# Performance work log

Hardware: AMD Instinct MI355X
Metric: run time of the kernel (lower is better)

The kernel has to match this reference:

```python
import jax, jax.numpy as jnp
import numpy as np

B, S, K, N, NO = 2, 4096, 4096, 4096, 32


def setup_inputs() -> dict:
    key = jax.random.key(0)
    k0, k1, k2, k3 = jax.random.split(key, 4)
    # activations with a few high-magnitude 'outlier' columns (LLM.int8-style)
    x = jax.random.normal(k0, (B, S, K), dtype=jnp.float16)
    ind = jnp.sort(jax.random.randint(k1, (NO,), 0, K)).astype(jnp.int32)
    x = x.at[:, :, ind].multiply(jnp.float16(30.0))
    # fp16 master weight -> quantize exactly as the module's init path does
    w = (jax.random.normal(k2, (N, K), dtype=jnp.float32) * 0.02)
    weight_cache = w[:, ind].astype(jnp.float16)          # original outlier cols
    w_z = w.at[:, ind].set(0.0)                            # zero outlier cols
    scale = (jnp.max(jnp.abs(w_z), axis=1) / 127.0)        # per-out-channel scale
    q_weight = jnp.clip(jnp.round(w_z / scale[:, None]), -128.0, 127.0).astype(jnp.int8)
    bias = (jax.random.normal(k3, (N,), dtype=jnp.float32) * 0.01)
    # packed (N, 2): [:, 0] = dequant scale, [:, 1] = bias (matches q_scale_col layout)
    scale_col = jnp.stack([scale, bias], axis=1).astype(jnp.float16)
    return {
        "x": x,
        "q_weight": q_weight,
        "scale_col": scale_col,
        "weight_cache": weight_cache,
        "ind": ind,
    }


def reference(x, q_weight, scale_col, weight_cache, ind):
    # mixgemmforward_dynamic: per-row dynamic activation quant, int8 GEMM,
    # per-(row,col) dequant, fused bias add, fp16 outlier-column correction.
    Bx, Sx, Kx = x.shape
    Nx = q_weight.shape[0]
    xf = x.astype(jnp.float32).reshape(-1, Kx)                    # [M, K]
    scale_row = jnp.max(jnp.abs(xf), axis=1, keepdims=True) / 127.0  # [M, 1]
    q_x = jnp.round(jnp.clip(xf / scale_row, -128.0, 127.0))      # int-valued f32
    acc = q_x @ q_weight.astype(jnp.float32).T                    # [M, N] int GEMM
    w_scale = scale_col[:, 0].astype(jnp.float32)                 # [N]
    bias = scale_col[:, 1].astype(jnp.float32)                    # [N]
    y = acc * scale_row * w_scale[None, :] + bias[None, :]
    # outlier correction: fp16 GEMM over the extracted outlier columns
    y = y + xf[:, ind] @ weight_cache.astype(jnp.float32).T
    return y.reshape(Bx, Sx, Nx).astype(jnp.float16)
```

## Files before the change

### kernel.cpp

```cpp
#include <hip/hip_runtime.h>
#include <stdint.h>


typedef float    f32x4  __attribute__((ext_vector_type(4)));
typedef int      i32x4  __attribute__((ext_vector_type(4)));
typedef _Float16 half8  __attribute__((ext_vector_type(8)));
typedef _Float16 half4  __attribute__((ext_vector_type(4)));

#define MTOT 8192
#define NTOT 4096
#define KTOT 4096

#define SWZ(r) (((r) >> 1) & 3)

static __device__ __forceinline__ void gload16(const int8_t* g, int8_t* l) {
  __builtin_amdgcn_global_load_lds(
      (const __attribute__((address_space(1))) void*)g,
      (__attribute__((address_space(3))) void*)l, 16, 0, 0);
}

__global__ __launch_bounds__(256) void pack_kernel(
    const int* __restrict__ qw32, int8_t* __restrict__ qw8,
    const float* __restrict__ wc, _Float16* __restrict__ wch)
{
  const int bid = blockIdx.x;
  const int t = threadIdx.x;
  if (bid < 4096) {
    const int base = bid * 4096;
#pragma unroll
    for (int g = 0; g < 4; ++g) {
      const int off = g * 1024 + t * 4;
      const i32x4 v = *(const i32x4*)(qw32 + base + off);
      const uint32_t o = (uint32_t)(v[0] & 255) | ((uint32_t)(v[1] & 255) << 8) |
                         ((uint32_t)(v[2] & 255) << 16) | ((uint32_t)(v[3] & 255) << 24);
      *(uint32_t*)(qw8 + base + off) = o;
    }
  } else {
    const int idx = (bid - 4096) * 1024 + t * 4;
    const float4 v = *(const float4*)(wc + idx);
    half4 h = {(_Float16)v.x, (_Float16)v.y, (_Float16)v.z, (_Float16)v.w};
    *(half4*)(wch + idx) = h;
  }
}

__global__ __launch_bounds__(256) void quant_kernel(
    const float* __restrict__ x, const int* __restrict__ ind,
    int8_t* __restrict__ qx, float* __restrict__ srow, _Float16* __restrict__ xo)
{
  const int t = threadIdx.x;
  const int w = t >> 6, l = t & 63;
  const int row = blockIdx.x * 4 + w;
  const float* xrow = x + (size_t)row * KTOT;
  const float4* xr = (const float4*)xrow;

  float4 v[16];
#pragma unroll
  for (int g = 0; g < 16; ++g) v[g] = xr[g * 64 + l];

  float am = 0.f;
#pragma unroll
  for (int g = 0; g < 16; ++g)
    am = fmaxf(am, fmaxf(fmaxf(fabsf(v[g].x), fabsf(v[g].y)),
                         fmaxf(fabsf(v[g].z), fabsf(v[g].w))));
#pragma unroll
  for (int off = 32; off; off >>= 1)
    am = fmaxf(am, __shfl_xor(am, off, 64));

  const float rscale = 127.0f / am;
  uint32_t* qrow = (uint32_t*)(qx + (size_t)row * KTOT);
#pragma unroll
  for (int g = 0; g < 16; ++g) {
    const float4 u = v[g];
    const int q0 = (int)rintf(fminf(fmaxf(u.x * rscale, -128.f), 127.f));
    const int q1 = (int)rintf(fminf(fmaxf(u.y * rscale, -128.f), 127.f));
    const int q2 = (int)rintf(fminf(fmaxf(u.z * rscale, -128.f), 127.f));
    const int q3 = (int)rintf(fminf(fmaxf(u.w * rscale, -128.f), 127.f));
    qrow[g * 64 + l] = (uint32_t)(q0 & 255) | ((uint32_t)(q1 & 255) << 8) |
                       ((uint32_t)(q2 & 255) << 16) | ((uint32_t)(q3 & 255) << 24);
  }
  if (l < 32) xo[row * 32 + l] = (_Float16)xrow[ind[l]];
  if (l == 0) srow[row] = am / 127.0f;
}

__global__ __launch_bounds__(256) void mixgemm_kernel(
    const int8_t* __restrict__ qx, const int8_t* __restrict__ qw,
    const float* __restrict__ srow, const float* __restrict__ sc,
    const _Float16* __restrict__ xo, const _Float16* __restrict__ wc,
    float* __restrict__ out)
{
  __shared__ int8_t lA[128 * 64];
  __shared__ int8_t lB[128 * 64];

  const int t = threadIdx.x;
  const int lane = t & 63;
  const int wid = t >> 6;
  const int wm = wid >> 1, wn = wid & 1;

  const int bid = blockIdx.x;
  const int swz = (bid & 7) * 256 + (bid >> 3);
  const int tn = swz & 31;
  const int tm = swz >> 5;
  const int bm0 = tm * 128, bn0 = tn * 128;

  const int rst = wid * 32 + (lane >> 2);
  const int cst = ((lane & 3) ^ SWZ(rst)) * 16;
  const int8_t* gA0 = qx + (size_t)(bm0 + rst) * KTOT + cst;
  const int8_t* gB0 = qw + (size_t)(bn0 + rst) * KTOT + cst;
  int8_t* dA = lA + wid * 2048;
  int8_t* dB = lB + wid * 2048;

  int roA[4], roB[4];
#pragma unroll
  for (int i = 0; i < 4; ++i) {
    const int ra = wm * 64 + i * 16 + (lane & 15);
    roA[i] = ra * 64 + (((lane >> 4) ^ SWZ(ra)) * 16);
    const int rb = wn * 64 + i * 16 + (lane & 15);
    roB[i] = rb * 64 + (((lane >> 4) ^ SWZ(rb)) * 16);
  }

  i32x4 acc[4][4];
#pragma unroll
  for (int i = 0; i < 4; ++i)
#pragma unroll
    for (int j = 0; j < 4; ++j) acc[i][j] = i32x4{0, 0, 0, 0};

  for (int kt = 0; kt < KTOT; kt += 64) {
    __syncthreads();
    gload16(gA0 + kt, dA);
    gload16(gA0 + kt + 16 * KTOT, dA + 1024);
    gload16(gB0 + kt, dB);
    gload16(gB0 + kt + 16 * KTOT, dB + 1024);
    __syncthreads();
    i32x4 af[4], bfr[4];
#pragma unroll
    for (int i = 0; i < 4; ++i) {
      af[i]  = *(const i32x4*)(lA + roA[i]);
      bfr[i] = *(const i32x4*)(lB + roB[i]);
    }
#pragma unroll
    for (int i = 0; i < 4; ++i)
#pragma unroll
      for (int j = 0; j < 4; ++j)
        acc[i][j] = __builtin_amdgcn_mfma_i32_16x16x64_i8(af[i], bfr[j], acc[i][j], 0, 0, 0);
  }

  {
    const int idx0 = t, idx1 = t + 256;
    const int r0 = idx0 >> 2, c0 = idx0 & 3;
    const int r1 = idx1 >> 2, c1 = idx1 & 3;
    const int w0 = r0 * 64 + ((c0 ^ SWZ(r0)) * 16);
    const int w1 = r1 * 64 + ((c1 ^ SWZ(r1)) * 16);
    const char* xob = (const char*)xo + (size_t)bm0 * 64;
    const char* wcb = (const char*)wc + (size_t)bn0 * 64;
    const i32x4 xs0 = *(const i32x4*)(xob + idx0 * 16);
    const i32x4 xs1 = *(const i32x4*)(xob + idx1 * 16);
    const i32x4 ws0 = *(const i32x4*)(wcb + idx0 * 16);
    const i32x4 ws1 = *(const i32x4*)(wcb + idx1 * 16);
    __syncthreads();
    *(i32x4*)(lA + w0) = xs0;
    *(i32x4*)(lA + w1) = xs1;
    *(i32x4*)(lB + w0) = ws0;
    *(i32x4*)(lB + w1) = ws1;
    __syncthreads();
  }
  f32x4 corr[4][4];
#pragma unroll
  for (int i = 0; i < 4; ++i)
#pragma unroll
    for (int j = 0; j < 4; ++j) corr[i][j] = f32x4{0.f, 0.f, 0.f, 0.f};
  {
    half8 xf[4], wf[4];
#pragma unroll
    for (int i = 0; i < 4; ++i) {
      xf[i] = __builtin_bit_cast(half8, *(const i32x4*)(lA + roA[i]));
      wf[i] = __builtin_bit_cast(half8, *(const i32x4*)(lB + roB[i]));
    }
#pragma unroll
    for (int i = 0; i < 4; ++i)
#pragma unroll
      for (int j = 0; j < 4; ++j)
        corr[i][j] = __builtin_amdgcn_mfma_f32_16x16x32_f16(xf[i], wf[j], corr[i][j], 0, 0, 0);
  }

#pragma unroll
  for (int i = 0; i < 4; ++i) {
    const int rowg = bm0 + wm * 64 + i * 16 + (lane >> 4) * 4;
    const f32x4 sr = *(const f32x4*)(srow + rowg);
#pragma unroll
    for (int j = 0; j < 4; ++j) {
      const int colg = bn0 + wn * 64 + j * 16 + (lane & 15);
      const float2 scb = ((const float2*)sc)[colg];
      float* op = out + (size_t)rowg * NTOT + colg;
#pragma unroll
      for (int r = 0; r < 4; ++r) {
        const float y = (float)acc[i][j][r] * (sr[r] * scb.x) + scb.y + corr[i][j][r];
        op[(size_t)r * NTOT] = y;
      }
    }
  }
}

extern "C" void kernel_launch(void* const* d_in, const int* in_sizes, int n_in,
                              void* d_out, int out_size, void* d_ws, size_t ws_size,
                              hipStream_t stream) {
  (void)in_sizes; (void)n_in; (void)out_size; (void)ws_size;
  const float* x    = (const float*)d_in[0];
  const int*   qw32 = (const int*)d_in[1];
  const float* sc   = (const float*)d_in[2];
  const float* wcf  = (const float*)d_in[3];
  const int*   ind  = (const int*)d_in[4];
  float* out = (float*)d_out;

  char* ws = (char*)d_ws;
  int8_t*   qx   = (int8_t*)ws;
  float*    srow = (float*)(ws + 33554432);
  _Float16* xo   = (_Float16*)(ws + 33587200);
  int8_t*   qw8  = (int8_t*)(ws + 34111488);
  _Float16* wch  = (_Float16*)(ws + 50888704);

  pack_kernel<<<4096 + 128, 256, 0, stream>>>(qw32, qw8, wcf, wch);
  quant_kernel<<<MTOT / 4, 256, 0, stream>>>(x, ind, qx, srow, xo);
  mixgemm_kernel<<<(MTOT / 128) * (NTOT / 128), 256, 0, stream>>>(qx, qw8, srow, sc, xo, wch, out);
}
```

Baseline: 446.9 us.

## Double-buffer LDS tiles in int8 GEMM and merge prep kernels into one launch

The GEMM main loop now uses two LDS buffers, so the next K-tile's global-to-LDS loads are issued while MFMAs run on the current tile. This cuts the loop from two barriers per iteration to one. Separately, the weight pack and activation quantization kernels are merged into a single prep launch, removing one launch and letting the two independent jobs run concurrently. Doubling LDS to 32KB per block may lower occupancy, and the single-barrier scheme relies on the direct-to-LDS loads being complete when the barrier is reached.

```diff
diff --git a/kernel.cpp b/kernel.cpp
--- a/kernel.cpp
+++ b/kernel.cpp
@@ -19,9 +19,12 @@
       (__attribute__((address_space(3))) void*)l, 16, 0, 0);
 }
 
-__global__ __launch_bounds__(256) void pack_kernel(
-    const int* __restrict__ qw32, int8_t* __restrict__ qw8,
-    const float* __restrict__ wc, _Float16* __restrict__ wch)
+__global__ __launch_bounds__(256) void prep_kernel(
+    const float* __restrict__ x, const int* __restrict__ ind,
+    const int* __restrict__ qw32,
+    int8_t* __restrict__ qx, float* __restrict__ srow, _Float16* __restrict__ xo,
+    int8_t* __restrict__ qw8, _Float16* __restrict__ wch,
+    const float* __restrict__ wc)
 {
   const int bid = blockIdx.x;
   const int t = threadIdx.x;
@@ -35,51 +38,45 @@
                          ((uint32_t)(v[2] & 255) << 16) | ((uint32_t)(v[3] & 255) << 24);
       *(uint32_t*)(qw8 + base + off) = o;
     }
-  } else {
+  } else if (bid < 4224) {
     const int idx = (bid - 4096) * 1024 + t * 4;
     const float4 v = *(const float4*)(wc + idx);
     half4 h = {(_Float16)v.x, (_Float16)v.y, (_Float16)v.z, (_Float16)v.w};
     *(half4*)(wch + idx) = h;
-  }
-}
-
-__global__ __launch_bounds__(256) void quant_kernel(
-    const float* __restrict__ x, const int* __restrict__ ind,
-    int8_t* __restrict__ qx, float* __restrict__ srow, _Float16* __restrict__ xo)
-{
-  const int t = threadIdx.x;
-  const int w = t >> 6, l = t & 63;
-  const int row = blockIdx.x * 4 + w;
-  const float* xrow = x + (size_t)row * KTOT;
-  const float4* xr = (const float4*)xrow;
-
-  float4 v[16];
-#pragma unroll
-  for (int g = 0; g < 16; ++g) v[g] = xr[g * 64 + l];
-
-  float am = 0.f;
-#pragma unroll
-  for (int g = 0; g < 16; ++g)
-    am = fmaxf(am, fmaxf(fmaxf(fabsf(v[g].x), fabsf(v[g].y)),
-                         fmaxf(fabsf(v[g].z), fabsf(v[g].w))));
-#pragma unroll
-  for (int off = 32; off; off >>= 1)
-    am = fmaxf(am, __shfl_xor(am, off, 64));
-
-  const float rscale = 127.0f / am;
-  uint32_t* qrow = (uint32_t*)(qx + (size_t)row * KTOT);
-#pragma unroll
-  for (int g = 0; g < 16; ++g) {
-    const float4 u = v[g];
-    const int q0 = (int)rintf(fminf(fmaxf(u.x * rscale, -128.f), 127.f));
-    const int q1 = (int)rintf(fminf(fmaxf(u.y * rscale, -128.f), 127.f));
-    const int q2 = (int)rintf(fminf(fmaxf(u.z * rscale, -128.f), 127.f));
-    const int q3 = (int)rintf(fminf(fmaxf(u.w * rscale, -128.f), 127.f));
-    qrow[g * 64 + l] = (uint32_t)(q0 & 255) | ((uint32_t)(q1 & 255) << 8) |
-                       ((uint32_t)(q2 & 255) << 16) | ((uint32_t)(q3 & 255) << 24);
-  }
-  if (l < 32) xo[row * 32 + l] = (_Float16)xrow[ind[l]];
-  if (l == 0) srow[row] = am / 127.0f;
+  } else {
+    const int w = t >> 6, l = t & 63;
+    const int row = (bid - 4224) * 4 + w;
+    const float* xrow = x + (size_t)row * KTOT;
+    const float4* xr = (const float4*)xrow;
+
+    float4 v[16];
+#pragma unroll
+    for (int g = 0; g < 16; ++g) v[g] = xr[g * 64 + l];
+
+    float am = 0.f;
+#pragma unroll
+    for (int g = 0; g < 16; ++g)
+      am = fmaxf(am, fmaxf(fmaxf(fabsf(v[g].x), fabsf(v[g].y)),
+                           fmaxf(fabsf(v[g].z), fabsf(v[g].w))));
+#pragma unroll
+    for (int off = 32; off; off >>= 1)
+      am = fmaxf(am, __shfl_xor(am, off, 64));
+
+    const float rscale = 127.0f / am;
+    uint32_t* qrow = (uint32_t*)(qx + (size_t)row * KTOT);
+#pragma unroll
+    for (int g = 0; g < 16; ++g) {
+      const float4 u = v[g];
+      const int q0 = (int)rintf(fminf(fmaxf(u.x * rscale, -128.f), 127.f));
+      const int q1 = (int)rintf(fminf(fmaxf(u.y * rscale, -128.f), 127.f));
+      const int q2 = (int)rintf(fminf(fmaxf(u.z * rscale, -128.f), 127.f));
+      const int q3 = (int)rintf(fminf(fmaxf(u.w * rscale, -128.f), 127.f));
+      qrow[g * 64 + l] = (uint32_t)(q0 & 255) | ((uint32_t)(q1 & 255) << 8) |
+                         ((uint32_t)(q2 & 255) << 16) | ((uint32_t)(q3 & 255) << 24);
+    }
+    if (l < 32) xo[row * 32 + l] = (_Float16)xrow[ind[l]];
+    if (l == 0) srow[row] = am / 127.0f;
+  }
 }
 
 __global__ __launch_bounds__(256) void mixgemm_kernel(
@@ -88,8 +85,8 @@
     const _Float16* __restrict__ xo, const _Float16* __restrict__ wc,
     float* __restrict__ out)
 {
-  __shared__ int8_t lA[128 * 64];
-  __shared__ int8_t lB[128 * 64];
+  __shared__ int8_t lA[2][8192];
+  __shared__ int8_t lB[2][8192];
 
   const int t = threadIdx.x;
   const int lane = t & 63;
@@ -106,8 +103,7 @@
   const int cst = ((lane & 3) ^ SWZ(rst)) * 16;
   const int8_t* gA0 = qx + (size_t)(bm0 + rst) * KTOT + cst;
   const int8_t* gB0 = qw + (size_t)(bn0 + rst) * KTOT + cst;
-  int8_t* dA = lA + wid * 2048;
-  int8_t* dB = lB + wid * 2048;
+  const int wo = wid * 2048;
 
   int roA[4], roB[4];
 #pragma unroll
@@ -124,18 +120,39 @@
 #pragma unroll
     for (int j = 0; j < 4; ++j) acc[i][j] = i32x4{0, 0, 0, 0};
 
-  for (int kt = 0; kt < KTOT; kt += 64) {
+  gload16(gA0, lA[0] + wo);
+  gload16(gA0 + 16 * KTOT, lA[0] + wo + 1024);
+  gload16(gB0, lB[0] + wo);
+  gload16(gB0 + 16 * KTOT, lB[0] + wo + 1024);
+  __syncthreads();
+
+  int cur = 0;
+  for (int kt = 64; kt < KTOT; kt += 64) {
+    const int nxt = cur ^ 1;
+    gload16(gA0 + kt, lA[nxt] + wo);
+    gload16(gA0 + kt + 16 * KTOT, lA[nxt] + wo + 1024);
+    gload16(gB0 + kt, lB[nxt] + wo);
+    gload16(gB0 + kt + 16 * KTOT, lB[nxt] + wo + 1024);
+    i32x4 af[4], bfr[4];
+#pragma unroll
+    for (int i = 0; i < 4; ++i) {
+      af[i]  = *(const i32x4*)(lA[cur] + roA[i]);
+      bfr[i] = *(const i32x4*)(lB[cur] + roB[i]);
+    }
+#pragma unroll
+    for (int i = 0; i < 4; ++i)
+#pragma unroll
+      for (int j = 0; j < 4; ++j)
+        acc[i][j] = __builtin_amdgcn_mfma_i32_16x16x64_i8(af[i], bfr[j], acc[i][j], 0, 0, 0);
     __syncthreads();
-    gload16(gA0 + kt, dA);
-    gload16(gA0 + kt + 16 * KTOT, dA + 1024);
-    gload16(gB0 + kt, dB);
-    gload16(gB0 + kt + 16 * KTOT, dB + 1024);
-    __syncthreads();
+    cur = nxt;
+  }
+  {
     i32x4 af[4], bfr[4];
 #pragma unroll
     for (int i = 0; i < 4; ++i) {
-      af[i]  = *(const i32x4*)(lA + roA[i]);
-      bfr[i] = *(const i32x4*)(lB + roB[i]);
+      af[i]  = *(const i32x4*)(lA[cur] + roA[i]);
+      bfr[i] = *(const i32x4*)(lB[cur] + roB[i]);
     }
 #pragma unroll
     for (int i = 0; i < 4; ++i)
@@ -157,10 +174,10 @@
     const i32x4 ws0 = *(const i32x4*)(wcb + idx0 * 16);
     const i32x4 ws1 = *(const i32x4*)(wcb + idx1 * 16);
     __syncthreads();
-    *(i32x4*)(lA + w0) = xs0;
-    *(i32x4*)(lA + w1) = xs1;
-    *(i32x4*)(lB + w0) = ws0;
-    *(i32x4*)(lB + w1) = ws1;
+    *(i32x4*)(lA[0] + w0) = xs0;
+    *(i32x4*)(lA[0] + w1) = xs1;
+    *(i32x4*)(lB[0] + w0) = ws0;
+    *(i32x4*)(lB[0] + w1) = ws1;
     __syncthreads();
   }
   f32x4 corr[4][4];
@@ -172,8 +189,8 @@
     half8 xf[4], wf[4];
 #pragma unroll
     for (int i = 0; i < 4; ++i) {
-      xf[i] = __builtin_bit_cast(half8, *(const i32x4*)(lA + roA[i]));
-      wf[i] = __builtin_bit_cast(half8, *(const i32x4*)(lB + roB[i]));
+      xf[i] = __builtin_bit_cast(half8, *(const i32x4*)(lA[0] + roA[i]));
+      wf[i] = __builtin_bit_cast(half8, *(const i32x4*)(lB[0] + roB[i]));
     }
 #pragma unroll
     for (int i = 0; i < 4; ++i)
@@ -218,7 +235,6 @@
   int8_t*   qw8  = (int8_t*)(ws + 34111488);
   _Float16* wch  = (_Float16*)(ws + 50888704);
 
-  pack_kernel<<<4096 + 128, 256, 0, stream>>>(qw32, qw8, wcf, wch);
-  quant_kernel<<<MTOT / 4, 256, 0, stream>>>(x, ind, qx, srow, xo);
+  prep_kernel<<<4224 + MTOT / 4, 256, 0, stream>>>(x, ind, qw32, qx, srow, xo, qw8, wch, wcf);
   mixgemm_kernel<<<(MTOT / 128) * (NTOT / 128), 256, 0, stream>>>(qx, qw8, srow, sc, xo, wch, out);
 }
```

Result: slower. 478.1 us (+7.0%).

## Double GEMM K-tile to 128 with 8-way swizzle and fuse prep kernels

Applied to the files above, without the earlier changes.

Merges the weight-pack and activation-quant kernels into a single launch to remove one kernel launch and its tail. Doubles the int8 GEMM K-step to 128 bytes per stage with a new 8-chunk XOR LDS swizzle, halving the number of barrier pairs per tile and issuing more loads per sync. LDS usage grows to 32 KB per block, which may reduce occupancy.

```diff
diff --git a/kernel.cpp b/kernel.cpp
--- a/kernel.cpp
+++ b/kernel.cpp
@@ -11,7 +11,7 @@
 #define NTOT 4096
 #define KTOT 4096
 
-#define SWZ(r) (((r) >> 1) & 3)
+#define SWZ4(r) (((r) >> 1) & 3)
 
 static __device__ __forceinline__ void gload16(const int8_t* g, int8_t* l) {
   __builtin_amdgcn_global_load_lds(
@@ -19,9 +19,12 @@
       (__attribute__((address_space(3))) void*)l, 16, 0, 0);
 }
 
-__global__ __launch_bounds__(256) void pack_kernel(
-    const int* __restrict__ qw32, int8_t* __restrict__ qw8,
-    const float* __restrict__ wc, _Float16* __restrict__ wch)
+__global__ __launch_bounds__(256) void prep_kernel(
+    const float* __restrict__ x, const int* __restrict__ ind,
+    const int* __restrict__ qw32,
+    int8_t* __restrict__ qx, float* __restrict__ srow, _Float16* __restrict__ xo,
+    int8_t* __restrict__ qw8, _Float16* __restrict__ wch,
+    const float* __restrict__ wc)
 {
   const int bid = blockIdx.x;
   const int t = threadIdx.x;
@@ -35,51 +38,45 @@
                          ((uint32_t)(v[2] & 255) << 16) | ((uint32_t)(v[3] & 255) << 24);
       *(uint32_t*)(qw8 + base + off) = o;
     }
-  } else {
+  } else if (bid < 4224) {
     const int idx = (bid - 4096) * 1024 + t * 4;
     const float4 v = *(const float4*)(wc + idx);
     half4 h = {(_Float16)v.x, (_Float16)v.y, (_Float16)v.z, (_Float16)v.w};
     *(half4*)(wch + idx) = h;
-  }
-}
-
-__global__ __launch_bounds__(256) void quant_kernel(
-    const float* __restrict__ x, const int* __restrict__ ind,
-    int8_t* __restrict__ qx, float* __restrict__ srow, _Float16* __restrict__ xo)
-{
-  const int t = threadIdx.x;
-  const int w = t >> 6, l = t & 63;
-  const int row = blockIdx.x * 4 + w;
-  const float* xrow = x + (size_t)row * KTOT;
-  const float4* xr = (const float4*)xrow;
-
-  float4 v[16];
-#pragma unroll
-  for (int g = 0; g < 16; ++g) v[g] = xr[g * 64 + l];
-
-  float am = 0.f;
-#pragma unroll
-  for (int g = 0; g < 16; ++g)
-    am = fmaxf(am, fmaxf(fmaxf(fabsf(v[g].x), fabsf(v[g].y)),
-                         fmaxf(fabsf(v[g].z), fabsf(v[g].w))));
-#pragma unroll
-  for (int off = 32; off; off >>= 1)
-    am = fmaxf(am, __shfl_xor(am, off, 64));
-
-  const float rscale = 127.0f / am;
-  uint32_t* qrow = (uint32_t*)(qx + (size_t)row * KTOT);
-#pragma unroll
-  for (int g = 0; g < 16; ++g) {
-    const float4 u = v[g];
-    const int q0 = (int)rintf(fminf(fmaxf(u.x * rscale, -128.f), 127.f));
-    const int q1 = (int)rintf(fminf(fmaxf(u.y * rscale, -128.f), 127.f));
-    const int q2 = (int)rintf(fminf(fmaxf(u.z * rscale, -128.f), 127.f));
-    const int q3 = (int)rintf(fminf(fmaxf(u.w * rscale, -128.f), 127.f));
-    qrow[g * 64 + l] = (uint32_t)(q0 & 255) | ((uint32_t)(q1 & 255) << 8) |
-                       ((uint32_t)(q2 & 255) << 16) | ((uint32_t)(q3 & 255) << 24);
-  }
-  if (l < 32) xo[row * 32 + l] = (_Float16)xrow[ind[l]];
-  if (l == 0) srow[row] = am / 127.0f;
+  } else {
+    const int w = t >> 6, l = t & 63;
+    const int row = (bid - 4224) * 4 + w;
+    const float* xrow = x + (size_t)row * KTOT;
+    const float4* xr = (const float4*)xrow;
+
+    float4 v[16];
+#pragma unroll
+    for (int g = 0; g < 16; ++g) v[g] = xr[g * 64 + l];
+
+    float am = 0.f;
+#pragma unroll
+    for (int g = 0; g < 16; ++g)
+      am = fmaxf(am, fmaxf(fmaxf(fabsf(v[g].x), fabsf(v[g].y)),
+                           fmaxf(fabsf(v[g].z), fabsf(v[g].w))));
+#pragma unroll
+    for (int off = 32; off; off >>= 1)
+      am = fmaxf(am, __shfl_xor(am, off, 64));
+
+    const float rscale = 127.0f / am;
+    uint32_t* qrow = (uint32_t*)(qx + (size_t)row * KTOT);
+#pragma unroll
+    for (int g = 0; g < 16; ++g) {
+      const float4 u = v[g];
+      const int q0 = (int)rintf(fminf(fmaxf(u.x * rscale, -128.f), 127.f));
+      const int q1 = (int)rintf(fminf(fmaxf(u.y * rscale, -128.f), 127.f));
+      const int q2 = (int)rintf(fminf(fmaxf(u.z * rscale, -128.f), 127.f));
+      const int q3 = (int)rintf(fminf(fmaxf(u.w * rscale, -128.f), 127.f));
+      qrow[g * 64 + l] = (uint32_t)(q0 & 255) | ((uint32_t)(q1 & 255) << 8) |
+                         ((uint32_t)(q2 & 255) << 16) | ((uint32_t)(q3 & 255) << 24);
+    }
+    if (l < 32) xo[row * 32 + l] = (_Float16)xrow[ind[l]];
+    if (l == 0) srow[row] = am / 127.0f;
+  }
 }
 
 __global__ __launch_bounds__(256) void mixgemm_kernel(
@@ -88,8 +85,8 @@
     const _Float16* __restrict__ xo, const _Float16* __restrict__ wc,
     float* __restrict__ out)
 {
-  __shared__ int8_t lA[128 * 64];
-  __shared__ int8_t lB[128 * 64];
+  __shared__ int8_t lA[128 * 128];
+  __shared__ int8_t lB[128 * 128];
 
   const int t = threadIdx.x;
   const int lane = t & 63;
@@ -102,20 +99,20 @@
   const int tm = swz >> 5;
   const int bm0 = tm * 128, bn0 = tn * 128;
 
-  const int rst = wid * 32 + (lane >> 2);
-  const int cst = ((lane & 3) ^ SWZ(rst)) * 16;
+  const int rst = wid * 32 + (lane >> 3);
+  const int cst = ((lane & 7) ^ (lane >> 3)) * 16;
   const int8_t* gA0 = qx + (size_t)(bm0 + rst) * KTOT + cst;
   const int8_t* gB0 = qw + (size_t)(bn0 + rst) * KTOT + cst;
-  int8_t* dA = lA + wid * 2048;
-  int8_t* dB = lB + wid * 2048;
+  int8_t* dA = lA + wid * 4096;
+  int8_t* dB = lB + wid * 4096;
 
   int roA[4], roB[4];
 #pragma unroll
   for (int i = 0; i < 4; ++i) {
     const int ra = wm * 64 + i * 16 + (lane & 15);
-    roA[i] = ra * 64 + (((lane >> 4) ^ SWZ(ra)) * 16);
+    roA[i] = ra * 128 + (((lane >> 4) ^ (ra & 7)) * 16);
     const int rb = wn * 64 + i * 16 + (lane & 15);
-    roB[i] = rb * 64 + (((lane >> 4) ^ SWZ(rb)) * 16);
+    roB[i] = rb * 128 + (((lane >> 4) ^ (rb & 7)) * 16);
   }
 
   i32x4 acc[4][4];
@@ -124,32 +121,37 @@
 #pragma unroll
     for (int j = 0; j < 4; ++j) acc[i][j] = i32x4{0, 0, 0, 0};
 
-  for (int kt = 0; kt < KTOT; kt += 64) {
-    __syncthreads();
-    gload16(gA0 + kt, dA);
-    gload16(gA0 + kt + 16 * KTOT, dA + 1024);
-    gload16(gB0 + kt, dB);
-    gload16(gB0 + kt + 16 * KTOT, dB + 1024);
-    __syncthreads();
-    i32x4 af[4], bfr[4];
-#pragma unroll
-    for (int i = 0; i < 4; ++i) {
-      af[i]  = *(const i32x4*)(lA + roA[i]);
-      bfr[i] = *(const i32x4*)(lB + roB[i]);
-    }
-#pragma unroll
-    for (int i = 0; i < 4; ++i)
-#pragma unroll
-      for (int j = 0; j < 4; ++j)
-        acc[i][j] = __builtin_amdgcn_mfma_i32_16x16x64_i8(af[i], bfr[j], acc[i][j], 0, 0, 0);
+  for (int kt = 0; kt < KTOT; kt += 128) {
+    __syncthreads();
+#pragma unroll
+    for (int s = 0; s < 4; ++s) {
+      gload16(gA0 + kt + (size_t)s * 8 * KTOT, dA + s * 1024);
+      gload16(gB0 + kt + (size_t)s * 8 * KTOT, dB + s * 1024);
+    }
+    __syncthreads();
+#pragma unroll
+    for (int kk = 0; kk < 2; ++kk) {
+      const int xk = kk * 64;
+      i32x4 af[4], bfr[4];
+#pragma unroll
+      for (int i = 0; i < 4; ++i) {
+        af[i]  = *(const i32x4*)(lA + (roA[i] ^ xk));
+        bfr[i] = *(const i32x4*)(lB + (roB[i] ^ xk));
+      }
+#pragma unroll
+      for (int i = 0; i < 4; ++i)
+#pragma unroll
+        for (int j = 0; j < 4; ++j)
+          acc[i][j] = __builtin_amdgcn_mfma_i32_16x16x64_i8(af[i], bfr[j], acc[i][j], 0, 0, 0);
+    }
   }
 
   {
     const int idx0 = t, idx1 = t + 256;
     const int r0 = idx0 >> 2, c0 = idx0 & 3;
     const int r1 = idx1 >> 2, c1 = idx1 & 3;
-    const int w0 = r0 * 64 + ((c0 ^ SWZ(r0)) * 16);
-    const int w1 = r1 * 64 + ((c1 ^ SWZ(r1)) * 16);
+    const int w0 = r0 * 64 + ((c0 ^ SWZ4(r0)) * 16);
+    const int w1 = r1 * 64 + ((c1 ^ SWZ4(r1)) * 16);
     const char* xob = (const char*)xo + (size_t)bm0 * 64;
     const char* wcb = (const char*)wc + (size_t)bn0 * 64;
     const i32x4 xs0 = *(const i32x4*)(xob + idx0 * 16);
@@ -172,8 +174,12 @@
     half8 xf[4], wf[4];
 #pragma unroll
     for (int i = 0; i < 4; ++i) {
-      xf[i] = __builtin_bit_cast(half8, *(const i32x4*)(lA + roA[i]));
-      wf[i] = __builtin_bit_cast(half8, *(const i32x4*)(lB + roB[i]));
+      const int ra = wm * 64 + i * 16 + (lane & 15);
+      const int rb = wn * 64 + i * 16 + (lane & 15);
+      const int oA = ra * 64 + (((lane >> 4) ^ SWZ4(ra)) * 16);
+      const int oB = rb * 64 + (((lane >> 4) ^ SWZ4(rb)) * 16);
+      xf[i] = __builtin_bit_cast(half8, *(const i32x4*)(lA + oA));
+      wf[i] = __builtin_bit_cast(half8, *(const i32x4*)(lB + oB));
     }
 #pragma unroll
     for (int i = 0; i < 4; ++i)
@@ -218,7 +224,6 @@
   int8_t*   qw8  = (int8_t*)(ws + 34111488);
   _Float16* wch  = (_Float16*)(ws + 50888704);
 
-  pack_kernel<<<4096 + 128, 256, 0, stream>>>(qw32, qw8, wcf, wch);
-  quant_kernel<<<MTOT / 4, 256, 0, stream>>>(x, ind, qx, srow, xo);
+  prep_kernel<<<4224 + MTOT / 4, 256, 0, stream>>>(x, ind, qw32, qx, srow, xo, qw8, wch, wcf);
   mixgemm_kernel<<<(MTOT / 128) * (NTOT / 128), 256, 0, stream>>>(qx, qw8, srow, sc, xo, wch, out);
 }
```

After: 425.8 us. 4.7% less time.
